# Performance work log

Hardware: AMD Instinct MI355X
Metric: run time of the kernel (lower is better)

Reference implementation:

```python
import jax, jax.numpy as jnp
import numpy as np

T = 16384
SIGMA = 0.1745
KAPPA = 1.0 / (SIGMA * SIGMA)  # ~32.84


def setup_inputs() -> dict:
    key = jax.random.key(0)
    ks = jax.random.split(key, 10)
    s = 0.05  # small init scale to keep tanh unsaturated
    return {
        "angle": jax.random.uniform(ks[0], (1, T, 1), dtype=jnp.float32) * 360.0,  # degrees
        "rule": jax.random.normal(ks[1], (1, T, 1), dtype=jnp.float32),
        "w_rule": jax.random.normal(ks[2], (128, 1), dtype=jnp.float32) * s,
        "b_rule": jax.random.normal(ks[3], (128,), dtype=jnp.float32) * s,
        "w_ih": jax.random.normal(ks[4], (361, 489), dtype=jnp.float32) * s,
        "w_hh": jax.random.normal(ks[5], (361, 361), dtype=jnp.float32) * s,
        "b_ih": jax.random.normal(ks[6], (361,), dtype=jnp.float32) * s,
        "b_hh": jax.random.normal(ks[7], (361,), dtype=jnp.float32) * s,
        "w_fc": jax.random.normal(ks[8], (1, 361), dtype=jnp.float32) * s,
        "b_fc": jax.random.normal(ks[9], (1,), dtype=jnp.float32) * s,
    }


def reference(angle, rule, w_rule, b_rule, w_ih, w_hh, b_ih, b_hh, w_fc, b_fc):
    # Vectorized von Mises PDF over the 0..360 degree grid (replaces scipy loop):
    # pdf(x) = exp(kappa*cos(x - mu)) / (2*pi*I0(kappa))
    grid = jnp.arange(361, dtype=jnp.float32) * (jnp.pi / 180.0)  # [361]
    mu = jnp.deg2rad(angle[0, :, 0])  # [T]
    norm = 2.0 * jnp.pi * jax.scipy.special.i0(jnp.float32(KAPPA))
    angle_input = jnp.exp(KAPPA * jnp.cos(grid[None, :] - mu[:, None])) / norm  # [T,361]

    rule_input = rule @ w_rule.T + b_rule  # [1,T,128]
    combined = jnp.concatenate([rule_input, angle_input[None]], axis=2)  # [1,T,489]

    # Single-layer tanh RNN (batch=1), zero initial hidden state.
    x = combined[0]  # [T,489]
    xw = x @ w_ih.T + (b_ih + b_hh)  # precompute input contribution [T,361]

    def step(h, xt):
        h = jnp.tanh(xt + h @ w_hh.T)
        return h, h

    h0 = jnp.zeros((361,), dtype=x.dtype)
    _, hs = jax.lax.scan(step, h0, xw)  # hs: [T,361]
    out = hs[None]  # [1,T,361]
    outcome_pre = out @ w_fc.T + b_fc  # [1,T,1]
    return outcome_pre, out
```

## Files before the change

kernel.cpp:

```cpp
#include <hip/hip_runtime.h>
#include <cmath>

#define T_STEPS 16384
#define NH 361
#define NIN 489
#define NRULE 128

typedef _Float16 half8 __attribute__((ext_vector_type(8)));
typedef float f32x4 __attribute__((ext_vector_type(4)));

static constexpr double PI_D = 3.14159265358979323846;

__global__ void k0_prep(const float* __restrict__ w_ih, const float* __restrict__ w_rule,
                        const float* __restrict__ b_rule, const float* __restrict__ b_ih,
                        const float* __restrict__ b_hh,
                        float* __restrict__ Av, float* __restrict__ Cv,
                        float* __restrict__ w2t) {
  int idx = blockIdx.x * 256 + threadIdx.x;
  if (idx < NH * NH) {
    int i = idx % NH;
    int j = idx / NH;
    w2t[idx] = w_ih[i * NIN + NRULE + j];
  }
  if (idx < NH) {
    float a = 0.f, c = 0.f;
    for (int k = 0; k < NRULE; ++k) {
      float w = w_ih[idx * NIN + k];
      a += w * w_rule[k];
      c += w * b_rule[k];
    }
    Av[idx] = a;
    Cv[idx] = c + b_ih[idx] + b_hh[idx];
  }
}

__global__ void k1_xw(const float* __restrict__ angle, const float* __restrict__ rule,
                      const float* __restrict__ Av, const float* __restrict__ Cv,
                      const float* __restrict__ w2t, float* __restrict__ xw,
                      float kappa, float vmS) {
  __shared__ float vm[NH][32];
  __shared__ float srule[32];
  const int tid = threadIdx.x;
  const int t0 = blockIdx.x * 32;
  const float DEG = (float)(PI_D / 180.0);

  for (int idx = tid; idx < NH * 32; idx += 256) {
    int j = idx >> 5;
    int tt = idx & 31;
    float mu = angle[t0 + tt] * DEG;
    float c = __cosf((float)j * DEG - mu);
    vm[j][tt] = vmS * __expf(kappa * (c - 1.f));
  }
  if (tid < 32) srule[tid] = rule[t0 + tid];
  __syncthreads();

  for (int i = tid; i < NH; i += 256) {
    float acc[32];
#pragma unroll
    for (int tt = 0; tt < 32; ++tt) acc[tt] = 0.f;
    for (int j = 0; j < NH; ++j) {
      float wv = w2t[j * NH + i];
#pragma unroll
      for (int tt = 0; tt < 32; ++tt) acc[tt] += wv * vm[j][tt];
    }
    float Ai = Av[i], Ci = Cv[i];
#pragma unroll
    for (int tt = 0; tt < 32; ++tt)
      xw[(t0 + tt) * NH + i] = acc[tt] + srule[tt] * Ai + Ci;
  }
}

__global__ __launch_bounds__(512, 2) void k2_rnn(const float* __restrict__ w_hh,
                                                 const float* __restrict__ xw,
                                                 float* __restrict__ hs) {
  __shared__ _Float16 afrag[2][12][64][8];
  const int tid = threadIdx.x;
  const int wv = tid >> 6;
  const int lane = tid & 63;
  const int l15 = lane & 15;
  const int lhi = lane >> 4;

  int* lp = (int*)&afrag[0][0][0][0];
  for (int idx = tid; idx < 6144; idx += 512) lp[idx] = 0;

  half8 bw[3][12];
#pragma unroll
  for (int ct = 0; ct < 3; ++ct) {
    const int i = (wv * 3 + ct) * 16 + l15;
#pragma unroll
    for (int kt = 0; kt < 12; ++kt) {
      half8 v;
#pragma unroll
      for (int e = 0; e < 8; ++e) {
        const int k = kt * 32 + lhi * 8 + e;
        float x = (i < NH && k < NH) ? w_hh[i * NH + k] : 0.f;
        v[e] = (_Float16)x;
      }
      bw[ct][kt] = v;
    }
  }

  const int ib = (wv * 3) * 16 + l15;
  float xwv0 = (ib < NH) ? xw[ib] : 0.f;
  float xwv1 = (ib + 16 < NH) ? xw[ib + 16] : 0.f;
  float xwv2 = (ib + 32 < NH) ? xw[ib + 32] : 0.f;
  __syncthreads();

  const f32x4 zero4 = {0.f, 0.f, 0.f, 0.f};
  for (int t = 0; t < T_STEPS; ++t) {
    const int tn = (t + 1 < T_STEPS) ? (t + 1) : t;
    const float* pn = xw + tn * NH;
    float xwn0 = (ib < NH) ? pn[ib] : 0.f;
    float xwn1 = (ib + 16 < NH) ? pn[ib + 16] : 0.f;
    float xwn2 = (ib + 32 < NH) ? pn[ib + 32] : 0.f;

    const _Float16* ab = &afrag[t & 1][0][0][0] + lane * 8;
    f32x4 aE0 = zero4, aE1 = zero4, aE2 = zero4;
    f32x4 aO0 = zero4, aO1 = zero4, aO2 = zero4;
    half8 a0 = *(const half8*)(ab);
    half8 a1 = *(const half8*)(ab + 512);
#pragma unroll
    for (int kt = 0; kt < 12; ++kt) {
      half8 an = (kt + 2 < 12) ? *(const half8*)(ab + (kt + 2) * 512) : a0;
      if (kt & 1) {
        aO0 = __builtin_amdgcn_mfma_f32_16x16x32_f16(a0, bw[0][kt], aO0, 0, 0, 0);
        aO1 = __builtin_amdgcn_mfma_f32_16x16x32_f16(a0, bw[1][kt], aO1, 0, 0, 0);
        aO2 = __builtin_amdgcn_mfma_f32_16x16x32_f16(a0, bw[2][kt], aO2, 0, 0, 0);
      } else {
        aE0 = __builtin_amdgcn_mfma_f32_16x16x32_f16(a0, bw[0][kt], aE0, 0, 0, 0);
        aE1 = __builtin_amdgcn_mfma_f32_16x16x32_f16(a0, bw[1][kt], aE1, 0, 0, 0);
        aE2 = __builtin_amdgcn_mfma_f32_16x16x32_f16(a0, bw[2][kt], aE2, 0, 0, 0);
      }
      a0 = a1; a1 = an;
    }

    float s0 = aE0[0] + aO0[0] + xwv0;
    float s1 = aE1[0] + aO1[0] + xwv1;
    float s2 = aE2[0] + aO2[0] + xwv2;
    float h0 = 1.f - __fdividef(2.f, __expf(2.f * s0) + 1.f);
    float h1 = 1.f - __fdividef(2.f, __expf(2.f * s1) + 1.f);
    float h2 = 1.f - __fdividef(2.f, __expf(2.f * s2) + 1.f);

    if (lane < 16) {
      float* orow = hs + (size_t)t * NH;
      _Float16* nb = &afrag[(t + 1) & 1][0][0][0];
      if (ib < NH) {
        orow[ib] = h0;
        nb[(ib >> 5) * 512 + ((ib >> 3) & 3) * 128 + (ib & 7)] = (_Float16)h0;
      }
      if (ib + 16 < NH) {
        int k = ib + 16;
        orow[k] = h1;
        nb[(k >> 5) * 512 + ((k >> 3) & 3) * 128 + (k & 7)] = (_Float16)h1;
      }
      if (ib + 32 < NH) {
        int k = ib + 32;
        orow[k] = h2;
        nb[(k >> 5) * 512 + ((k >> 3) & 3) * 128 + (k & 7)] = (_Float16)h2;
      }
    }
    xwv0 = xwn0; xwv1 = xwn1; xwv2 = xwn2;
    __syncthreads();
  }
}

__global__ void k3_fc(const float* __restrict__ hs, const float* __restrict__ w_fc,
                      const float* __restrict__ b_fc, float* __restrict__ out0) {
  const int t = blockIdx.x * 4 + (threadIdx.x >> 6);
  const int lane = threadIdx.x & 63;
  const float* hrow = hs + (size_t)t * NH;
  float s = 0.f;
  for (int j = lane; j < NH; j += 64) s += w_fc[j] * hrow[j];
#pragma unroll
  for (int off = 32; off > 0; off >>= 1) s += __shfl_down(s, off, 64);
  if (lane == 0) out0[t] = s + b_fc[0];
}

extern "C" void kernel_launch(void* const* d_in, const int* in_sizes, int n_in,
                              void* d_out, int out_size, void* d_ws, size_t ws_size,
                              hipStream_t stream) {
  const float* angle  = (const float*)d_in[0];
  const float* rule   = (const float*)d_in[1];
  const float* w_rule = (const float*)d_in[2];
  const float* b_rule = (const float*)d_in[3];
  const float* w_ih   = (const float*)d_in[4];
  const float* w_hh   = (const float*)d_in[5];
  const float* b_ih   = (const float*)d_in[6];
  const float* b_hh   = (const float*)d_in[7];
  const float* w_fc   = (const float*)d_in[8];
  const float* b_fc   = (const float*)d_in[9];
  float* out = (float*)d_out;

  float* xw  = (float*)d_ws;
  float* Av  = xw + (size_t)T_STEPS * NH;
  float* Cv  = Av + NH;
  float* w2t = Cv + NH;

  const double kappa = 1.0 / (0.1745 * 0.1745);
  double series = 1.0, term = 1.0;
  for (int k = 1; k < 16; ++k) {
    term *= ((2.0 * k - 1.0) * (2.0 * k - 1.0)) / (8.0 * kappa * (double)k);
    series += term;
  }
  const float vmS = (float)(sqrt(kappa / (2.0 * PI_D)) / series);

  k0_prep<<<(NH * NH + 255) / 256, 256, 0, stream>>>(w_ih, w_rule, b_rule, b_ih, b_hh,
                                                     Av, Cv, w2t);
  k1_xw<<<T_STEPS / 32, 256, 0, stream>>>(angle, rule, Av, Cv, w2t, xw,
                                          (float)kappa, vmS);
  k2_rnn<<<1, 512, 0, stream>>>(w_hh, xw, out + T_STEPS);
  k3_fc<<<T_STEPS / 4, 256, 0, stream>>>(out + T_STEPS, w_fc, b_fc, out);
}
```

Measured before the change: 15.39 ms.

## Replace MFMA recurrence with per-thread fdot2 matvec split over two threads per row

The serial RNN kernel now assigns each hidden unit to a pair of threads (768 threads total). Each thread holds half of its W_hh row in registers as fp16 and computes the dot product with packed fdot2 instructions, reading the broadcast hidden vector from LDS and combining the two halves with a lane shuffle. This drops the MFMA tile path, which wasted most of each 16x16 output tile on a batch-1 matvec and needed scattered fragment writes. The aim is a shorter per-step critical path, in exchange for more threads per barrier and a larger register footprint per thread.

```diff
diff --git a/kernel.cpp b/kernel.cpp
--- a/kernel.cpp
+++ b/kernel.cpp
@@ -7,7 +7,7 @@
 #define NRULE 128
 
 typedef _Float16 half8 __attribute__((ext_vector_type(8)));
-typedef float f32x4 __attribute__((ext_vector_type(4)));
+typedef _Float16 half2v __attribute__((ext_vector_type(2)));
 
 static constexpr double PI_D = 3.14159265358979323846;
 
@@ -70,96 +70,90 @@
   }
 }
 
-__global__ __launch_bounds__(512, 2) void k2_rnn(const float* __restrict__ w_hh,
+#define KHALF 192
+#define HSTRIDE 208
+
+__device__ inline float dot8(half8 a, half8 b, float acc) {
+  acc = __builtin_amdgcn_fdot2(__builtin_shufflevector(a, a, 0, 1),
+                               __builtin_shufflevector(b, b, 0, 1), acc, false);
+  acc = __builtin_amdgcn_fdot2(__builtin_shufflevector(a, a, 2, 3),
+                               __builtin_shufflevector(b, b, 2, 3), acc, false);
+  acc = __builtin_amdgcn_fdot2(__builtin_shufflevector(a, a, 4, 5),
+                               __builtin_shufflevector(b, b, 4, 5), acc, false);
+  acc = __builtin_amdgcn_fdot2(__builtin_shufflevector(a, a, 6, 7),
+                               __builtin_shufflevector(b, b, 6, 7), acc, false);
+  return acc;
+}
+
+__global__ __launch_bounds__(768, 3) void k2_rnn(const float* __restrict__ w_hh,
                                                  const float* __restrict__ xw,
                                                  float* __restrict__ hs) {
-  __shared__ _Float16 afrag[2][12][64][8];
+  __shared__ __align__(16) _Float16 hbuf[2][2 * HSTRIDE];
   const int tid = threadIdx.x;
-  const int wv = tid >> 6;
-  const int lane = tid & 63;
-  const int l15 = lane & 15;
-  const int lhi = lane >> 4;
-
-  int* lp = (int*)&afrag[0][0][0][0];
-  for (int idx = tid; idx < 6144; idx += 512) lp[idx] = 0;
-
-  half8 bw[3][12];
-#pragma unroll
-  for (int ct = 0; ct < 3; ++ct) {
-    const int i = (wv * 3 + ct) * 16 + l15;
-#pragma unroll
-    for (int kt = 0; kt < 12; ++kt) {
-      half8 v;
-#pragma unroll
-      for (int e = 0; e < 8; ++e) {
-        const int k = kt * 32 + lhi * 8 + e;
-        float x = (i < NH && k < NH) ? w_hh[i * NH + k] : 0.f;
-        v[e] = (_Float16)x;
+  const int i = tid >> 1;
+  const int kh = tid & 1;
+  const bool act = (i < NH);
+
+  for (int idx = tid; idx < 4 * HSTRIDE; idx += 768)
+    ((_Float16*)hbuf)[idx] = (_Float16)0.f;
+
+  half8 w[24];
+#pragma unroll
+  for (int c = 0; c < 24; ++c) {
+    half8 v;
+#pragma unroll
+    for (int e = 0; e < 8; ++e) {
+      const int k = kh * KHALF + c * 8 + e;
+      float x = (act && k < NH) ? w_hh[i * NH + k] : 0.f;
+      v[e] = (_Float16)x;
+    }
+    w[c] = v;
+  }
+
+  float xwv = act ? xw[i] : 0.f;
+  __syncthreads();
+
+  for (int t = 0; t < T_STEPS; ++t) {
+    const _Float16* hb = &hbuf[t & 1][kh * HSTRIDE];
+
+    half8 c0 = *(const half8*)(hb);
+    half8 c1 = *(const half8*)(hb + 8);
+    half8 c2 = *(const half8*)(hb + 16);
+    half8 c3 = *(const half8*)(hb + 24);
+
+    const int tn = (t + 1 < T_STEPS) ? (t + 1) : t;
+    float xwn = act ? xw[(size_t)tn * NH + i] : 0.f;
+
+    float a0 = 0.f, a1 = 0.f, a2 = 0.f, a3 = 0.f;
+#pragma unroll
+    for (int g = 0; g < 6; ++g) {
+      half8 n0 = c0, n1 = c1, n2 = c2, n3 = c3;
+      if (g < 5) {
+        const _Float16* p = hb + (g + 1) * 32;
+        n0 = *(const half8*)(p);
+        n1 = *(const half8*)(p + 8);
+        n2 = *(const half8*)(p + 16);
+        n3 = *(const half8*)(p + 24);
       }
-      bw[ct][kt] = v;
-    }
-  }
-
-  const int ib = (wv * 3) * 16 + l15;
-  float xwv0 = (ib < NH) ? xw[ib] : 0.f;
-  float xwv1 = (ib + 16 < NH) ? xw[ib + 16] : 0.f;
-  float xwv2 = (ib + 32 < NH) ? xw[ib + 32] : 0.f;
-  __syncthreads();
-
-  const f32x4 zero4 = {0.f, 0.f, 0.f, 0.f};
-  for (int t = 0; t < T_STEPS; ++t) {
-    const int tn = (t + 1 < T_STEPS) ? (t + 1) : t;
-    const float* pn = xw + tn * NH;
-    float xwn0 = (ib < NH) ? pn[ib] : 0.f;
-    float xwn1 = (ib + 16 < NH) ? pn[ib + 16] : 0.f;
-    float xwn2 = (ib + 32 < NH) ? pn[ib + 32] : 0.f;
-
-    const _Float16* ab = &afrag[t & 1][0][0][0] + lane * 8;
-    f32x4 aE0 = zero4, aE1 = zero4, aE2 = zero4;
-    f32x4 aO0 = zero4, aO1 = zero4, aO2 = zero4;
-    half8 a0 = *(const half8*)(ab);
-    half8 a1 = *(const half8*)(ab + 512);
-#pragma unroll
-    for (int kt = 0; kt < 12; ++kt) {
-      half8 an = (kt + 2 < 12) ? *(const half8*)(ab + (kt + 2) * 512) : a0;
-      if (kt & 1) {
-        aO0 = __builtin_amdgcn_mfma_f32_16x16x32_f16(a0, bw[0][kt], aO0, 0, 0, 0);
-        aO1 = __builtin_amdgcn_mfma_f32_16x16x32_f16(a0, bw[1][kt], aO1, 0, 0, 0);
-        aO2 = __builtin_amdgcn_mfma_f32_16x16x32_f16(a0, bw[2][kt], aO2, 0, 0, 0);
-      } else {
-        aE0 = __builtin_amdgcn_mfma_f32_16x16x32_f16(a0, bw[0][kt], aE0, 0, 0, 0);
-        aE1 = __builtin_amdgcn_mfma_f32_16x16x32_f16(a0, bw[1][kt], aE1, 0, 0, 0);
-        aE2 = __builtin_amdgcn_mfma_f32_16x16x32_f16(a0, bw[2][kt], aE2, 0, 0, 0);
-      }
-      a0 = a1; a1 = an;
-    }
-
-    float s0 = aE0[0] + aO0[0] + xwv0;
-    float s1 = aE1[0] + aO1[0] + xwv1;
-    float s2 = aE2[0] + aO2[0] + xwv2;
-    float h0 = 1.f - __fdividef(2.f, __expf(2.f * s0) + 1.f);
-    float h1 = 1.f - __fdividef(2.f, __expf(2.f * s1) + 1.f);
-    float h2 = 1.f - __fdividef(2.f, __expf(2.f * s2) + 1.f);
-
-    if (lane < 16) {
-      float* orow = hs + (size_t)t * NH;
-      _Float16* nb = &afrag[(t + 1) & 1][0][0][0];
-      if (ib < NH) {
-        orow[ib] = h0;
-        nb[(ib >> 5) * 512 + ((ib >> 3) & 3) * 128 + (ib & 7)] = (_Float16)h0;
-      }
-      if (ib + 16 < NH) {
-        int k = ib + 16;
-        orow[k] = h1;
-        nb[(k >> 5) * 512 + ((k >> 3) & 3) * 128 + (k & 7)] = (_Float16)h1;
-      }
-      if (ib + 32 < NH) {
-        int k = ib + 32;
-        orow[k] = h2;
-        nb[(k >> 5) * 512 + ((k >> 3) & 3) * 128 + (k & 7)] = (_Float16)h2;
-      }
-    }
-    xwv0 = xwn0; xwv1 = xwn1; xwv2 = xwn2;
+      a0 = dot8(c0, w[g * 4 + 0], a0);
+      a1 = dot8(c1, w[g * 4 + 1], a1);
+      a2 = dot8(c2, w[g * 4 + 2], a2);
+      a3 = dot8(c3, w[g * 4 + 3], a3);
+      c0 = n0; c1 = n1; c2 = n2; c3 = n3;
+    }
+
+    float s = (a0 + a1) + (a2 + a3);
+    s += __shfl_xor(s, 1, 64);
+
+    if (act && kh == 0) {
+      s += xwv;
+      const float e = __expf(2.f * s);
+      const float h = 1.f - __fdividef(2.f, e + 1.f);
+      hs[(size_t)t * NH + i] = h;
+      const int di = (i < KHALF) ? i : (HSTRIDE + i - KHALF);
+      hbuf[(t + 1) & 1][di] = (_Float16)h;
+    }
+    xwv = xwn;
     __syncthreads();
   }
 }
@@ -208,6 +202,6 @@
                                                      Av, Cv, w2t);
   k1_xw<<<T_STEPS / 32, 256, 0, stream>>>(angle, rule, Av, Cv, w2t, xw,
                                           (float)kappa, vmS);
-  k2_rnn<<<1, 512, 0, stream>>>(w_hh, xw, out + T_STEPS);
+  k2_rnn<<<1, 768, 0, stream>>>(w_hh, xw, out + T_STEPS);
   k3_fc<<<T_STEPS / 4, 256, 0, stream>>>(out + T_STEPS, w_fc, b_fc, out);
 }
```

After: 15.34 ms. Within noise of the previous version (-0.3%).

## Replace MFMA matvec in RNN loop with fdot2 and DPP reductions

Applied to the files above, without the earlier changes.

The recurrent kernel drops the 16x16x32 MFMA formulation, which wasted most of the tile on a batch-1 matvec, in favour of per-thread packed fp16 dot products (v_dot2). Each group of 8 lanes owns 6 output rows and reduces its partial sums with DPP row shuffles. The hidden state now lives in a flat 384-element LDS buffer instead of a swizzled MFMA fragment layout. This is meant to shorten per-step latency on the serial critical path, at the cost of more VALU work and a 3-level DPP reduction per step.

```diff
diff --git a/kernel.cpp b/kernel.cpp
--- a/kernel.cpp
+++ b/kernel.cpp
@@ -7,7 +7,7 @@
 #define NRULE 128
 
 typedef _Float16 half8 __attribute__((ext_vector_type(8)));
-typedef float f32x4 __attribute__((ext_vector_type(4)));
+typedef _Float16 h2_t __attribute__((ext_vector_type(2)));
 
 static constexpr double PI_D = 3.14159265358979323846;
 
@@ -70,96 +70,104 @@
   }
 }
 
+union H8 {
+  half8 v8;
+  h2_t h2[4];
+};
+
+template <int CTRL>
+__device__ __forceinline__ float dpp_add(float x) {
+  int m = __builtin_amdgcn_update_dpp(0, __float_as_int(x), CTRL, 0xF, 0xF, true);
+  return x + __int_as_float(m);
+}
+
 __global__ __launch_bounds__(512, 2) void k2_rnn(const float* __restrict__ w_hh,
                                                  const float* __restrict__ xw,
                                                  float* __restrict__ hs) {
-  __shared__ _Float16 afrag[2][12][64][8];
+  __shared__ __align__(16) _Float16 hbuf[2][384];
   const int tid = threadIdx.x;
-  const int wv = tid >> 6;
-  const int lane = tid & 63;
-  const int l15 = lane & 15;
-  const int lhi = lane >> 4;
-
-  int* lp = (int*)&afrag[0][0][0][0];
-  for (int idx = tid; idx < 6144; idx += 512) lp[idx] = 0;
-
-  half8 bw[3][12];
-#pragma unroll
-  for (int ct = 0; ct < 3; ++ct) {
-    const int i = (wv * 3 + ct) * 16 + l15;
-#pragma unroll
-    for (int kt = 0; kt < 12; ++kt) {
-      half8 v;
+  const int g = tid >> 3;
+  const int s = tid & 7;
+
+  for (int idx = tid; idx < 768; idx += 512)
+    ((_Float16*)hbuf)[idx] = (_Float16)0.f;
+
+  H8 wt[6][6];
+#pragma unroll
+  for (int r = 0; r < 6; ++r) {
+    const int i = r * 64 + g;
+#pragma unroll
+    for (int c = 0; c < 6; ++c) {
 #pragma unroll
       for (int e = 0; e < 8; ++e) {
-        const int k = kt * 32 + lhi * 8 + e;
+        const int k = s * 48 + c * 8 + e;
         float x = (i < NH && k < NH) ? w_hh[i * NH + k] : 0.f;
-        v[e] = (_Float16)x;
+        wt[r][c].v8[e] = (_Float16)x;
       }
-      bw[ct][kt] = v;
-    }
-  }
-
-  const int ib = (wv * 3) * 16 + l15;
-  float xwv0 = (ib < NH) ? xw[ib] : 0.f;
-  float xwv1 = (ib + 16 < NH) ? xw[ib + 16] : 0.f;
-  float xwv2 = (ib + 32 < NH) ? xw[ib + 32] : 0.f;
+    }
+  }
+
+  float xwv[6];
+  if (s == 0) {
+#pragma unroll
+    for (int r = 0; r < 6; ++r) {
+      const int i = r * 64 + g;
+      xwv[r] = (i < NH) ? xw[i] : 0.f;
+    }
+  }
   __syncthreads();
 
-  const f32x4 zero4 = {0.f, 0.f, 0.f, 0.f};
   for (int t = 0; t < T_STEPS; ++t) {
+    const _Float16* hb = &hbuf[t & 1][s * 48];
+    H8 hc[6];
+#pragma unroll
+    for (int c = 0; c < 6; ++c) hc[c].v8 = *(const half8*)(hb + c * 8);
+
     const int tn = (t + 1 < T_STEPS) ? (t + 1) : t;
-    const float* pn = xw + tn * NH;
-    float xwn0 = (ib < NH) ? pn[ib] : 0.f;
-    float xwn1 = (ib + 16 < NH) ? pn[ib + 16] : 0.f;
-    float xwn2 = (ib + 32 < NH) ? pn[ib + 32] : 0.f;
-
-    const _Float16* ab = &afrag[t & 1][0][0][0] + lane * 8;
-    f32x4 aE0 = zero4, aE1 = zero4, aE2 = zero4;
-    f32x4 aO0 = zero4, aO1 = zero4, aO2 = zero4;
-    half8 a0 = *(const half8*)(ab);
-    half8 a1 = *(const half8*)(ab + 512);
-#pragma unroll
-    for (int kt = 0; kt < 12; ++kt) {
-      half8 an = (kt + 2 < 12) ? *(const half8*)(ab + (kt + 2) * 512) : a0;
-      if (kt & 1) {
-        aO0 = __builtin_amdgcn_mfma_f32_16x16x32_f16(a0, bw[0][kt], aO0, 0, 0, 0);
-        aO1 = __builtin_amdgcn_mfma_f32_16x16x32_f16(a0, bw[1][kt], aO1, 0, 0, 0);
-        aO2 = __builtin_amdgcn_mfma_f32_16x16x32_f16(a0, bw[2][kt], aO2, 0, 0, 0);
-      } else {
-        aE0 = __builtin_amdgcn_mfma_f32_16x16x32_f16(a0, bw[0][kt], aE0, 0, 0, 0);
-        aE1 = __builtin_amdgcn_mfma_f32_16x16x32_f16(a0, bw[1][kt], aE1, 0, 0, 0);
-        aE2 = __builtin_amdgcn_mfma_f32_16x16x32_f16(a0, bw[2][kt], aE2, 0, 0, 0);
+    float xwn[6];
+    if (s == 0) {
+      const float* pn = xw + (size_t)tn * NH;
+#pragma unroll
+      for (int r = 0; r < 6; ++r) {
+        const int i = r * 64 + g;
+        xwn[r] = (i < NH) ? pn[i] : 0.f;
       }
-      a0 = a1; a1 = an;
-    }
-
-    float s0 = aE0[0] + aO0[0] + xwv0;
-    float s1 = aE1[0] + aO1[0] + xwv1;
-    float s2 = aE2[0] + aO2[0] + xwv2;
-    float h0 = 1.f - __fdividef(2.f, __expf(2.f * s0) + 1.f);
-    float h1 = 1.f - __fdividef(2.f, __expf(2.f * s1) + 1.f);
-    float h2 = 1.f - __fdividef(2.f, __expf(2.f * s2) + 1.f);
-
-    if (lane < 16) {
+    }
+
+    float ps[6] = {0.f, 0.f, 0.f, 0.f, 0.f, 0.f};
+#pragma unroll
+    for (int c = 0; c < 6; ++c)
+#pragma unroll
+      for (int j = 0; j < 4; ++j)
+#pragma unroll
+        for (int r = 0; r < 6; ++r)
+          ps[r] = __builtin_amdgcn_fdot2(hc[c].h2[j], wt[r][c].h2[j], ps[r], false);
+
+#pragma unroll
+    for (int r = 0; r < 6; ++r) {
+      float v = ps[r];
+      v = dpp_add<0xB1>(v);
+      v = dpp_add<0x4E>(v);
+      v = dpp_add<0x104>(v);
+      ps[r] = v;
+    }
+
+    if (s == 0) {
       float* orow = hs + (size_t)t * NH;
-      _Float16* nb = &afrag[(t + 1) & 1][0][0][0];
-      if (ib < NH) {
-        orow[ib] = h0;
-        nb[(ib >> 5) * 512 + ((ib >> 3) & 3) * 128 + (ib & 7)] = (_Float16)h0;
+      _Float16* nb = hbuf[(t + 1) & 1];
+#pragma unroll
+      for (int r = 0; r < 6; ++r) {
+        const int i = r * 64 + g;
+        if (i < NH) {
+          const float sv = ps[r] + xwv[r];
+          const float e = __expf(2.f * sv);
+          const float h = 1.f - __fdividef(2.f, e + 1.f);
+          orow[i] = h;
+          nb[i] = (_Float16)h;
+        }
+        xwv[r] = xwn[r];
       }
-      if (ib + 16 < NH) {
-        int k = ib + 16;
-        orow[k] = h1;
-        nb[(k >> 5) * 512 + ((k >> 3) & 3) * 128 + (k & 7)] = (_Float16)h1;
-      }
-      if (ib + 32 < NH) {
-        int k = ib + 32;
-        orow[k] = h2;
-        nb[(k >> 5) * 512 + ((k >> 3) & 3) * 128 + (k & 7)] = (_Float16)h2;
-      }
-    }
-    xwv0 = xwn0; xwv1 = xwn1; xwv2 = xwn2;
+    }
     __syncthreads();
   }
 }
```

Result: slower. 25.64 ms (+66.6%).
